# Kernel tuning notes

Hardware: AMD Instinct MI355X
Metric: run time of the kernel (lower is better)

The kernel has to match this reference:

```python
import jax, jax.numpy as jnp
import numpy as np

B, S, T, D, H, HID, V, O = 8, 512, 256, 768, 12, 3072, 50257, 64
HD = D // H  # head dim = 64


def setup_inputs() -> dict:
    key = jax.random.key(0)
    ks = jax.random.split(key, 20)
    s = 0.02
    return {
        'source_input_ids': jax.random.randint(ks[0], (B, S), 0, V, dtype=jnp.int32),
        'encoder_hidden_states': jax.random.normal(ks[1], (B, S, D), dtype=jnp.float32),
        'encoder_attn_mask': jnp.zeros((B, S), dtype=bool),
        'decoder_hidden_states': jax.random.normal(ks[2], (B, T, D), dtype=jnp.float32),
        'onto_ids': jnp.arange(V - O, V, dtype=jnp.int32),
        # MultiheadAttention params (torch layout: W [out,in])
        'Wq': jax.random.normal(ks[3], (D, D)) * s, 'bq': jnp.zeros((D,)),
        'Wk': jax.random.normal(ks[4], (D, D)) * s, 'bk': jnp.zeros((D,)),
        'Wv': jax.random.normal(ks[5], (D, D)) * s, 'bv': jnp.zeros((D,)),
        'Wo': jax.random.normal(ks[6], (D, D)) * s, 'bo': jnp.zeros((D,)),
        # CopyHead: Linear(D, 1)
        'copy_w': jax.random.normal(ks[7], (D, 1)) * s, 'copy_b': jnp.zeros((1,)),
        # Generator FFN: Linear(D, HID) -> relu -> Linear(HID, O)
        'W1': jax.random.normal(ks[8], (HID, D)) * s, 'b1': jnp.zeros((HID,)),
        'W2': jax.random.normal(ks[9], (O, HID)) * s, 'b2': jnp.zeros((O,)),
    }


def _forward(source_input_ids, encoder_hidden_states, encoder_attn_mask,
             decoder_hidden_states, onto_ids, Wq, bq, Wk, bk, Wv, bv, Wo, bo,
             copy_w, copy_b, W1, b1, W2, b2):
    # ---- Generator: FFN + softmax over ontology vocab ----
    h = jax.nn.relu(decoder_hidden_states @ W1.T + b1)
    ontology_probs = jax.nn.softmax(h @ W2.T + b2, axis=-1)  # [B,T,O]

    # ---- MultiheadAttention (batch_first, eval: no dropout) ----
    q = (decoder_hidden_states @ Wq.T + bq).reshape(B, T, H, HD)
    k = (encoder_hidden_states @ Wk.T + bk).reshape(B, S, H, HD)
    v = (encoder_hidden_states @ Wv.T + bv).reshape(B, S, H, HD)
    scores = jnp.einsum('bthd,bshd->bhts', q, k) / jnp.sqrt(jnp.float32(HD))
    scores = jnp.where(encoder_attn_mask[:, None, None, :], -jnp.inf, scores)
    attn = jax.nn.softmax(scores, axis=-1)                       # [B,H,T,S]
    ctx = jnp.einsum('bhts,bshd->bthd', attn, v).reshape(B, T, D)
    context_outputs = ctx @ Wo.T + bo                            # [B,T,D]
    from_source_probs = attn.mean(axis=1)                        # avg heads [B,T,S]

    # ---- CopyHead ----
    copy_probs = jax.nn.sigmoid(context_outputs @ copy_w + copy_b)  # [B,T,1]

    from_source_probs = from_source_probs * copy_probs
    ontology_probs = ontology_probs * (1.0 - copy_probs)

    # ---- scatter-add into full vocab distribution ----
    bi = jnp.arange(B)[:, None, None]
    ti = jnp.arange(T)[None, :, None]
    vocab_probs = jnp.zeros((B, T, V), dtype=copy_probs.dtype)
    vocab_probs = vocab_probs.at[bi, ti, source_input_ids[:, None, :]].add(from_source_probs)
    vocab_probs = vocab_probs.at[bi, ti, onto_ids[None, None, :]].add(ontology_probs)
    return vocab_probs


def reference(source_input_ids, encoder_hidden_states, encoder_attn_mask,
              decoder_hidden_states, onto_ids, Wq, bq, Wk, bk, Wv, bv, Wo, bo,
              copy_w, copy_b, W1, b1, W2, b2):
    return _forward(source_input_ids, encoder_hidden_states, encoder_attn_mask,
                    decoder_hidden_states, onto_ids, Wq, bq, Wk, bk, Wv, bv,
                    Wo, bo, copy_w, copy_b, W1, b1, W2, b2)
```

## Files before the change

kernel.cpp:

```cpp
#include <hip/hip_runtime.h>
#include <hip/hip_bf16.h>
#include <math.h>

constexpr int B = 8, S = 512, T = 256, D = 768, H = 12, HID = 3072;
constexpr int V = 50257, O = 64, HD = 64;

typedef short bf16x8 __attribute__((ext_vector_type(8)));
typedef float f32x4 __attribute__((ext_vector_type(4)));

__device__ __forceinline__ float b2f(unsigned short u) {
  union { float f; unsigned v; } x; x.v = ((unsigned)u) << 16; return x.f;
}
__device__ __forceinline__ unsigned short f2b(float f) {
  __hip_bfloat16 h = __float2bfloat16(f);
  return *(unsigned short*)&h;
}

__device__ __forceinline__ void async16(const void* g, void* l) {
  __builtin_amdgcn_global_load_lds(
      (const __attribute__((address_space(1))) void*)g,
      (__attribute__((address_space(3))) void*)l, 16, 0, 0);
}

constexpr int CH0 = B * T * D / 8;
constexpr int CH1 = CH0 + B * S * D / 8;
constexpr int CH2 = CH1 + HID * D / 8;
constexpr int CH3 = CH2 + D * D / 8;
constexpr int CH4 = CH3 + D * D / 8;
constexpr int CH5 = CH4 + D * D / 8;
constexpr int CH6 = CH5 + O * HID / 8;

__global__ void cvt_weff_kernel(
    const float* __restrict__ dec, const float* __restrict__ enc,
    const float* __restrict__ W1, const float* __restrict__ Wq,
    const float* __restrict__ Wk, const float* __restrict__ Wv,
    const float* __restrict__ W2, const float* __restrict__ Wo,
    const float* __restrict__ bo, const float* __restrict__ cw,
    const float* __restrict__ cb,
    __hip_bfloat16* __restrict__ decb, __hip_bfloat16* __restrict__ encb,
    __hip_bfloat16* __restrict__ WA, __hip_bfloat16* __restrict__ WB,
    __hip_bfloat16* __restrict__ W2b, float* __restrict__ weff) {
  int i = blockIdx.x * blockDim.x + threadIdx.x;
  if (i >= CH6) {
    int j = i - CH6;
    if (j < D) {
      float acc = 0.f;
      for (int o = 0; o < D; ++o) acc += Wo[(size_t)o * D + j] * cw[o];
      weff[j] = acc;
    } else if (j == D) {
      float acc = cb[0];
      for (int o = 0; o < D; ++o) acc += bo[o] * cw[o];
      weff[D] = acc;
    }
    return;
  }
  const float* src;
  __hip_bfloat16* dst;
  int j;
  if (i < CH0)      { src = dec; dst = decb;                 j = i; }
  else if (i < CH1) { src = enc; dst = encb;                 j = i - CH0; }
  else if (i < CH2) { src = W1;  dst = WA;                   j = i - CH1; }
  else if (i < CH3) { src = Wq;  dst = WA + (size_t)HID * D; j = i - CH2; }
  else if (i < CH4) { src = Wk;  dst = WB;                   j = i - CH3; }
  else if (i < CH5) { src = Wv;  dst = WB + (size_t)D * D;   j = i - CH4; }
  else              { src = W2;  dst = W2b;                  j = i - CH5; }
  size_t e = (size_t)j * 8;
  float4 v0 = *(const float4*)&src[e];
  float4 v1 = *(const float4*)&src[e + 4];
  ushort4 o0, o1;
  o0.x = f2b(v0.x); o0.y = f2b(v0.y); o0.z = f2b(v0.z); o0.w = f2b(v0.w);
  o1.x = f2b(v1.x); o1.y = f2b(v1.y); o1.z = f2b(v1.z); o1.w = f2b(v1.w);
  *(ushort4*)&dst[e] = o0;
  *(ushort4*)&dst[e + 4] = o1;
}

__device__ __forceinline__ void zero_range(float* out, long long lo4,
                                           long long hi4, int zb, int nzb) {
  f32x4* o4 = (f32x4*)out;
  const f32x4 z = {0.f, 0.f, 0.f, 0.f};
  for (long long i = lo4 + (long long)zb * 256 + threadIdx.x; i < hi4;
       i += (long long)nzb * 256)
    __builtin_nontemporal_store(z, &o4[i]);
}

constexpr long long OUT_N4 = (long long)B * T * V / 4;
constexpr long long HALF4 = OUT_N4 / 2;

template <int BN, int MODE>
__device__ __forceinline__ void gemm_body(
    const __hip_bfloat16* __restrict__ A, const __hip_bfloat16* __restrict__ W,
    const float* __restrict__ bias0, const float* __restrict__ bias1,
    float* __restrict__ Cf, __hip_bfloat16* __restrict__ out0,
    __hip_bfloat16* __restrict__ out1, int M, int N, int K,
    int bx, int by, int kbeg, int kend,
    __hip_bfloat16* Als, __hip_bfloat16* Bls) {
  constexpr int BK = 32;
  constexpr int WTN = BN / 2;
  constexpr int NFRAG = WTN / 16;
  const int tid = threadIdx.x;
  const int lane = tid & 63, wid = tid >> 6;
  const int wm = wid >> 1, wn = wid & 1;
  const int row0 = by * 128, col0 = bx * BN;
  const int lr = lane & 15;
  const int ko = (lane >> 4) * 8;

  f32x4 acc[4][NFRAG] = {};

  for (int k0 = kbeg; k0 < kend; k0 += BK) {
#pragma unroll
    for (int c = 0; c < 2; ++c) {
      int j = tid + c * 256;
      int r = j >> 2, col = (j & 3) * 8;
      async16(&A[(size_t)(row0 + r) * K + k0 + col], (void*)&Als[j * 8]);
    }
#pragma unroll
    for (int c = 0; c < BN / 64; ++c) {
      int j = tid + c * 256;
      int r = j >> 2, col = (j & 3) * 8;
      async16(&W[(size_t)(col0 + r) * K + k0 + col], (void*)&Bls[j * 8]);
    }
    __syncthreads();

    bf16x8 af[4], bfr[NFRAG];
#pragma unroll
    for (int mi = 0; mi < 4; ++mi)
      af[mi] = *(const bf16x8*)&Als[(wm * 64 + mi * 16 + lr) * BK + ko];
#pragma unroll
    for (int ni = 0; ni < NFRAG; ++ni)
      bfr[ni] = *(const bf16x8*)&Bls[(wn * WTN + ni * 16 + lr) * BK + ko];
#pragma unroll
    for (int mi = 0; mi < 4; ++mi)
#pragma unroll
      for (int ni = 0; ni < NFRAG; ++ni)
        acc[mi][ni] = __builtin_amdgcn_mfma_f32_16x16x32_bf16(
            af[mi], bfr[ni], acc[mi][ni], 0, 0, 0);
    __syncthreads();
  }

#pragma unroll
  for (int mi = 0; mi < 4; ++mi) {
    int rbase = row0 + wm * 64 + mi * 16 + (lane >> 4) * 4;
#pragma unroll
    for (int ni = 0; ni < NFRAG; ++ni) {
      int c = col0 + wn * WTN + ni * 16 + lr;
#pragma unroll
      for (int r = 0; r < 4; ++r) {
        int rr = rbase + r;
        float a = acc[mi][ni][r];
        if constexpr (MODE == 1) {
          if (c < HID) {
            out0[(size_t)rr * HID + c] = __float2bfloat16(fmaxf(a + bias0[c], 0.f));
          } else {
            out1[(size_t)rr * D + (c - HID)] = __float2bfloat16(a + bias1[c - HID]);
          }
        } else if constexpr (MODE == 2) {
          if (c < D) {
            out0[(size_t)rr * D + c] = __float2bfloat16(a + bias0[c]);
          } else {
            int d = c - D;
            size_t idx = (((size_t)(rr >> 9) * D + d) << 9) | (size_t)(rr & 511);
            out1[idx] = __float2bfloat16(a + bias1[d]);
          }
        } else {
          Cf[(size_t)rr * N + c] = a;
        }
      }
    }
  }
}

constexpr int KV_BX = (2 * D) / 128;
constexpr int KV_BLOCKS = KV_BX * (B * S / 128);
constexpr int FQ_BX = (HID + D) / 128;
constexpr int FQ_BLOCKS = FQ_BX * (B * T / 128);
constexpr int GEMM_BLOCKS = KV_BLOCKS + FQ_BLOCKS;
constexpr int Z1 = 1024;

__global__ __launch_bounds__(256) void gemm_mega_kernel(
    const __hip_bfloat16* __restrict__ encb, const __hip_bfloat16* __restrict__ WB,
    const float* __restrict__ bk, const float* __restrict__ bv,
    __hip_bfloat16* __restrict__ kb16, __hip_bfloat16* __restrict__ vt,
    const __hip_bfloat16* __restrict__ decb, const __hip_bfloat16* __restrict__ WA,
    const float* __restrict__ b1, const float* __restrict__ bq,
    __hip_bfloat16* __restrict__ hb16, __hip_bfloat16* __restrict__ qb16,
    float* __restrict__ out) {
  __shared__ __hip_bfloat16 Als[128 * 32];
  __shared__ __hip_bfloat16 Bls[128 * 32];
  int bid = blockIdx.x;
  if (bid < KV_BLOCKS) {
    gemm_body<128, 2>(encb, WB, bk, bv, nullptr, kb16, vt,
                      B * S, 2 * D, D, bid % KV_BX, bid / KV_BX, 0, D, Als, Bls);
  } else if (bid < GEMM_BLOCKS) {
    int r = bid - KV_BLOCKS;
    gemm_body<128, 1>(decb, WA, b1, bq, nullptr, hb16, qb16,
                      B * T, HID + D, D, r % FQ_BX, r / FQ_BX, 0, D, Als, Bls);
  } else {
    zero_range(out, 0, HALF4, bid - GEMM_BLOCKS, Z1);
  }
}

constexpr int NSPLIT = 16;
constexpr int KCH = HID / NSPLIT;
constexpr int FFN2_BLOCKS = NSPLIT * (B * T / 128);

constexpr int ATTN_BLOCKS = B * H * (T / 32);
constexpr int Z2 = 1024;

__device__ void attn_body(
    const __hip_bfloat16* __restrict__ q, const __hip_bfloat16* __restrict__ k,
    const __hip_bfloat16* __restrict__ vt, const unsigned char* __restrict__ mask,
    __hip_bfloat16* __restrict__ ctx, __hip_bfloat16* __restrict__ Pg,
    int bid, char* smem) {
  constexpr int TB = 32;
  constexpr int SCP = 520;
  __hip_bfloat16* Qls = (__hip_bfloat16*)smem;
  __hip_bfloat16* KVls = Qls + TB * 64;
  __hip_bfloat16* sc = KVls + 128 * 64;
  const int tid = threadIdx.x;
  const int lane = tid & 63, w = tid >> 6;
  const int lr = lane & 15, lg = lane >> 4;
  const int tile = bid & 7;
  const int h = (bid >> 3) % H;
  const int b = bid / (8 * H);
  const int t0 = tile * TB;

  {
    int r = tid >> 3, slot = tid & 7;
    int g = slot ^ (r & 7);
    async16(&q[((size_t)(b * T + t0 + r)) * D + h * 64 + g * 8],
            (void*)&Qls[tid * 8]);
  }

  for (int ch = 0; ch < 4; ++ch) {
    const int s0 = ch * 128;
#pragma unroll
    for (int it = 0; it < 4; ++it) {
      int c = tid + it * 256;
      int r = c >> 3, slot = c & 7;
      int g = slot ^ (r & 7);
      async16(&k[((size_t)(b * S + s0 + r)) * D + h * 64 + g * 8],
              (void*)&KVls[c * 8]);
    }
    __syncthreads();
    f32x4 acc[2][2] = {};
#pragma unroll
    for (int ks = 0; ks < 2; ++ks) {
      bf16x8 af[2], bfr[2];
#pragma unroll
      for (int mi = 0; mi < 2; ++mi) {
        int row = mi * 16 + lr;
        int slot = (4 * ks + lg) ^ (row & 7);
        af[mi] = *(const bf16x8*)&Qls[row * 64 + slot * 8];
      }
#pragma unroll
      for (int ni = 0; ni < 2; ++ni) {
        int row = w * 32 + ni * 16 + lr;
        int slot = (4 * ks + lg) ^ (row & 7);
        bfr[ni] = *(const bf16x8*)&KVls[row * 64 + slot * 8];
      }
#pragma unroll
      for (int mi = 0; mi < 2; ++mi)
#pragma unroll
        for (int ni = 0; ni < 2; ++ni)
          acc[mi][ni] = __builtin_amdgcn_mfma_f32_16x16x32_bf16(
              af[mi], bfr[ni], acc[mi][ni], 0, 0, 0);
    }
#pragma unroll
    for (int ni = 0; ni < 2; ++ni) {
      int s_local = w * 32 + ni * 16 + lr;
      bool msk = mask[b * S + s0 + s_local];
#pragma unroll
      for (int mi = 0; mi < 2; ++mi) {
        int trow = mi * 16 + lg * 4;
#pragma unroll
        for (int rg = 0; rg < 4; ++rg) {
          float val = msk ? -INFINITY : acc[mi][ni][rg] * 0.125f;
          sc[(trow + rg) * SCP + s0 + s_local] = __float2bfloat16(val);
        }
      }
    }
    __syncthreads();
  }

  unsigned short* scu = (unsigned short*)sc;
  unsigned short* pgu = (unsigned short*)Pg;
#pragma unroll
  for (int i = 0; i < 8; ++i) {
    int r = w * 8 + i;
    float x[8];
    float m = -INFINITY;
#pragma unroll
    for (int j = 0; j < 8; ++j) {
      x[j] = b2f(scu[r * SCP + j * 64 + lane]);
      m = fmaxf(m, x[j]);
    }
#pragma unroll
    for (int o = 32; o > 0; o >>= 1) m = fmaxf(m, __shfl_xor(m, o));
    float ssum = 0.f;
#pragma unroll
    for (int j = 0; j < 8; ++j) { x[j] = __expf(x[j] - m); ssum += x[j]; }
#pragma unroll
    for (int o = 32; o > 0; o >>= 1) ssum += __shfl_xor(ssum, o);
    float inv = 1.f / ssum;
#pragma unroll
    for (int j = 0; j < 8; ++j) {
      unsigned short pb = f2b(x[j] * inv);
      scu[r * SCP + j * 64 + lane] = pb;
      pgu[(((size_t)(b * H + h)) * T + t0 + r) * S + j * 64 + lane] = pb;
    }
  }
  __syncthreads();

  f32x4 accp[2] = {};
  for (int ch = 0; ch < 4; ++ch) {
    const int s0 = ch * 128;
#pragma unroll
    for (int it = 0; it < 4; ++it) {
      int c = tid + it * 256;
      int d = c >> 4, slot = c & 15;
      int g = slot ^ (d & 7);
      async16(&vt[(((size_t)(b * H + h)) * 64 + d) * S + s0 + g * 8],
              (void*)&KVls[c * 8]);
    }
    __syncthreads();
#pragma unroll
    for (int ks = 0; ks < 4; ++ks) {
      bf16x8 bfr;
      {
        int brow = w * 16 + lr;
        int slot = (4 * ks + lg) ^ (brow & 7);
        bfr = *(const bf16x8*)&KVls[brow * 128 + slot * 8];
      }
#pragma unroll
      for (int mi = 0; mi < 2; ++mi) {
        int prow = mi * 16 + lr;
        bf16x8 af = *(const bf16x8*)&sc[prow * SCP + s0 + ks * 32 + lg * 8];
        accp[mi] = __builtin_amdgcn_mfma_f32_16x16x32_bf16(af, bfr, accp[mi], 0, 0, 0);
      }
    }
    __syncthreads();
  }
#pragma unroll
  for (int mi = 0; mi < 2; ++mi) {
    int trow = mi * 16 + lg * 4;
#pragma unroll
    for (int rg = 0; rg < 4; ++rg) {
      ctx[((size_t)(b * T + t0 + trow + rg)) * D + h * 64 + w * 16 + lr] =
          __float2bfloat16(accp[mi][rg]);
    }
  }
}

__global__ __launch_bounds__(256) void attn_ffn2_kernel(
    const __hip_bfloat16* __restrict__ q, const __hip_bfloat16* __restrict__ k,
    const __hip_bfloat16* __restrict__ vt, const unsigned char* __restrict__ mask,
    __hip_bfloat16* __restrict__ ctx, __hip_bfloat16* __restrict__ Pg,
    const __hip_bfloat16* __restrict__ hb16, const __hip_bfloat16* __restrict__ W2b,
    float* __restrict__ part, float* __restrict__ out) {
  __shared__ __align__(16) char smem[53760];
  int bid = blockIdx.x;
  if (bid < ATTN_BLOCKS) {
    attn_body(q, k, vt, mask, ctx, Pg, bid, smem);
  } else if (bid < ATTN_BLOCKS + FFN2_BLOCKS) {
    int r = bid - ATTN_BLOCKS;
    int sp = r & (NSPLIT - 1), mt = r / NSPLIT;
    __hip_bfloat16* Als = (__hip_bfloat16*)smem;
    __hip_bfloat16* Bls = Als + 128 * 32;
    gemm_body<64, 3>(hb16, W2b, nullptr, nullptr,
                     part + (size_t)sp * (B * T) * 64, nullptr, nullptr,
                     B * T, 64, HID, 0, mt, sp * KCH, (sp + 1) * KCH, Als, Bls);
  } else {
    zero_range(out, HALF4, OUT_N4, bid - ATTN_BLOCKS - FFN2_BLOCKS, Z2);
  }
}

__global__ __launch_bounds__(256) void scatter3_kernel(
    const int* __restrict__ src, const int* __restrict__ onto,
    const __hip_bfloat16* __restrict__ Pg, const float* __restrict__ part,
    const float* __restrict__ b2v, const __hip_bfloat16* __restrict__ ctx,
    const float* __restrict__ weff, float* __restrict__ out) {
  const int bt = blockIdx.x;
  const int b = bt >> 8, t = bt & (T - 1);
  const int tid = threadIdx.x;
  const int lane = tid & 63;
  float* row = out + (size_t)bt * V;

  __shared__ float red[256];
  __shared__ float onts[O];

  const unsigned short* cu = (const unsigned short*)ctx + (size_t)bt * D;
  float a = 0.f;
#pragma unroll
  for (int j = 0; j < 3; ++j) {
    int d = j * 256 + tid;
    a += b2f(cu[d]) * weff[d];
  }
  red[tid] = a;
  __syncthreads();
  for (int st = 128; st > 0; st >>= 1) {
    if (tid < st) red[tid] += red[tid + st];
    __syncthreads();
  }
  const float cpv = 1.f / (1.f + __expf(-(red[0] + weff[D])));
  __syncthreads();

  if (tid < 64) {
    float x = b2v[lane];
#pragma unroll
    for (int sp = 0; sp < NSPLIT; ++sp)
      x += part[((size_t)sp * (B * T) + bt) * 64 + lane];
    float m = x;
#pragma unroll
    for (int o = 32; o > 0; o >>= 1) m = fmaxf(m, __shfl_xor(m, o));
    float e = __expf(x - m);
    float ss = e;
#pragma unroll
    for (int o = 32; o > 0; o >>= 1) ss += __shfl_xor(ss, o);
    onts[lane] = e / ss * (1.f - cpv);
  }
  __syncthreads();

  const unsigned short* pg = (const unsigned short*)Pg;
#pragma unroll
  for (int jj = 0; jj < 2; ++jj) {
    int s = jj * 256 + tid;
    float sum = 0.f;
#pragma unroll
    for (int h = 0; h < H; ++h)
      sum += b2f(pg[(((size_t)(b * H + h)) * T + t) * S + s]);
    atomicAdd(&row[src[b * S + s]], sum * (1.0f / (float)H) * cpv);
  }
  if (tid < O) atomicAdd(&row[onto[tid]], onts[tid]);
}

extern "C" void kernel_launch(void* const* d_in, const int* in_sizes, int n_in,
                              void* d_out, int out_size, void* d_ws, size_t ws_size,
                              hipStream_t stream) {
  const int* src_ids = (const int*)d_in[0];
  const float* enc = (const float*)d_in[1];
  const unsigned char* mask = (const unsigned char*)d_in[2];
  const float* dec = (const float*)d_in[3];
  const int* onto_ids = (const int*)d_in[4];
  const float* Wq = (const float*)d_in[5];
  const float* bq = (const float*)d_in[6];
  const float* Wk = (const float*)d_in[7];
  const float* bk = (const float*)d_in[8];
  const float* Wv = (const float*)d_in[9];
  const float* bv = (const float*)d_in[10];
  const float* Wo = (const float*)d_in[11];
  const float* bo = (const float*)d_in[12];
  const float* copy_w = (const float*)d_in[13];
  const float* copy_b = (const float*)d_in[14];
  const float* W1 = (const float*)d_in[15];
  const float* b1 = (const float*)d_in[16];
  const float* W2 = (const float*)d_in[17];
  const float* b2 = (const float*)d_in[18];

  const int MT = B * T;
  const int MS = B * S;

  __hip_bfloat16* wb = (__hip_bfloat16*)d_ws;
  __hip_bfloat16* qb16 = wb;    wb += (size_t)MT * D;
  __hip_bfloat16* kb16 = wb;    wb += (size_t)MS * D;
  __hip_bfloat16* vt = wb;      wb += (size_t)MS * D;
  __hip_bfloat16* ctxb16 = wb;  wb += (size_t)MT * D;
  __hip_bfloat16* W2b = wb;     wb += (size_t)O * HID;
  __hip_bfloat16* WB = wb;      wb += (size_t)2 * D * D;
  __hip_bfloat16* WA = wb;      wb += (size_t)(HID + D) * D;
  __hip_bfloat16* hb16 = wb;    wb += (size_t)MT * HID;
  __hip_bfloat16* Pg = wb;
  __hip_bfloat16* decb = wb;
  __hip_bfloat16* encb = decb + (size_t)MT * D;
  wb += (size_t)B * H * T * S;
  float* wf = (float*)wb;
  float* part = wf;             wf += (size_t)NSPLIT * MT * O;
  float* weff = wf;             wf += (size_t)(D + 1);

  float* out = (float*)d_out;

  cvt_weff_kernel<<<CH6 / 256 + 4, 256, 0, stream>>>(
      dec, enc, W1, Wq, Wk, Wv, W2, Wo, bo, copy_w, copy_b,
      decb, encb, WA, WB, W2b, weff);

  gemm_mega_kernel<<<GEMM_BLOCKS + Z1, 256, 0, stream>>>(
      encb, WB, bk, bv, kb16, vt, decb, WA, b1, bq, hb16, qb16, out);

  attn_ffn2_kernel<<<ATTN_BLOCKS + FFN2_BLOCKS + Z2, 256, 0, stream>>>(
      qb16, kb16, vt, mask, ctxb16, Pg, hb16, W2b, part, out);

  scatter3_kernel<<<MT, 256, 0, stream>>>(
      src_ids, onto_ids, Pg, part, b2, ctxb16, weff, out);
}
```

Measured before the change: 282.7 us.

## Move output zeroing into scatter kernel and swizzle block order for XCD locality

The output is no longer zeroed by extra blocks appended to the GEMM and attention kernels. Each scatter block now zeroes its own vocab row just before scattering into it, so that row is written while still warm in cache. The GEMM and attention block indices are remapped with an XCD-style swizzle so that neighbouring tiles land on the same chiplet and share its L2. FFN2 blocks are also moved ahead of attention in the launch order. The risk is that the zeroing, about 400 MB of stores, now sits on the scatter kernel's critical path instead of overlapping with compute, and the stores are no longer nontemporal.

```diff
diff --git a/kernel.cpp b/kernel.cpp
--- a/kernel.cpp
+++ b/kernel.cpp
@@ -74,18 +74,6 @@
   *(ushort4*)&dst[e + 4] = o1;
 }
 
-__device__ __forceinline__ void zero_range(float* out, long long lo4,
-                                           long long hi4, int zb, int nzb) {
-  f32x4* o4 = (f32x4*)out;
-  const f32x4 z = {0.f, 0.f, 0.f, 0.f};
-  for (long long i = lo4 + (long long)zb * 256 + threadIdx.x; i < hi4;
-       i += (long long)nzb * 256)
-    __builtin_nontemporal_store(z, &o4[i]);
-}
-
-constexpr long long OUT_N4 = (long long)B * T * V / 4;
-constexpr long long HALF4 = OUT_N4 / 2;
-
 template <int BN, int MODE>
 __device__ __forceinline__ void gemm_body(
     const __hip_bfloat16* __restrict__ A, const __hip_bfloat16* __restrict__ W,
@@ -174,7 +162,6 @@
 constexpr int FQ_BX = (HID + D) / 128;
 constexpr int FQ_BLOCKS = FQ_BX * (B * T / 128);
 constexpr int GEMM_BLOCKS = KV_BLOCKS + FQ_BLOCKS;
-constexpr int Z1 = 1024;
 
 __global__ __launch_bounds__(256) void gemm_mega_kernel(
     const __hip_bfloat16* __restrict__ encb, const __hip_bfloat16* __restrict__ WB,
@@ -182,20 +169,18 @@
     __hip_bfloat16* __restrict__ kb16, __hip_bfloat16* __restrict__ vt,
     const __hip_bfloat16* __restrict__ decb, const __hip_bfloat16* __restrict__ WA,
     const float* __restrict__ b1, const float* __restrict__ bq,
-    __hip_bfloat16* __restrict__ hb16, __hip_bfloat16* __restrict__ qb16,
-    float* __restrict__ out) {
+    __hip_bfloat16* __restrict__ hb16, __hip_bfloat16* __restrict__ qb16) {
   __shared__ __hip_bfloat16 Als[128 * 32];
   __shared__ __hip_bfloat16 Bls[128 * 32];
   int bid = blockIdx.x;
-  if (bid < KV_BLOCKS) {
+  int gid = (bid & 7) * (GEMM_BLOCKS / 8) + (bid >> 3);
+  if (gid < KV_BLOCKS) {
     gemm_body<128, 2>(encb, WB, bk, bv, nullptr, kb16, vt,
-                      B * S, 2 * D, D, bid % KV_BX, bid / KV_BX, 0, D, Als, Bls);
-  } else if (bid < GEMM_BLOCKS) {
-    int r = bid - KV_BLOCKS;
+                      B * S, 2 * D, D, gid % KV_BX, gid / KV_BX, 0, D, Als, Bls);
+  } else {
+    int r = gid - KV_BLOCKS;
     gemm_body<128, 1>(decb, WA, b1, bq, nullptr, hb16, qb16,
                       B * T, HID + D, D, r % FQ_BX, r / FQ_BX, 0, D, Als, Bls);
-  } else {
-    zero_range(out, 0, HALF4, bid - GEMM_BLOCKS, Z1);
   }
 }
 
@@ -204,7 +189,6 @@
 constexpr int FFN2_BLOCKS = NSPLIT * (B * T / 128);
 
 constexpr int ATTN_BLOCKS = B * H * (T / 32);
-constexpr int Z2 = 1024;
 
 __device__ void attn_body(
     const __hip_bfloat16* __restrict__ q, const __hip_bfloat16* __restrict__ k,
@@ -356,25 +340,24 @@
     const __hip_bfloat16* __restrict__ vt, const unsigned char* __restrict__ mask,
     __hip_bfloat16* __restrict__ ctx, __hip_bfloat16* __restrict__ Pg,
     const __hip_bfloat16* __restrict__ hb16, const __hip_bfloat16* __restrict__ W2b,
-    float* __restrict__ part, float* __restrict__ out) {
+    float* __restrict__ part) {
   __shared__ __align__(16) char smem[53760];
   int bid = blockIdx.x;
-  if (bid < ATTN_BLOCKS) {
-    attn_body(q, k, vt, mask, ctx, Pg, bid, smem);
-  } else if (bid < ATTN_BLOCKS + FFN2_BLOCKS) {
-    int r = bid - ATTN_BLOCKS;
-    int sp = r & (NSPLIT - 1), mt = r / NSPLIT;
+  if (bid < FFN2_BLOCKS) {
+    int sp = bid & (NSPLIT - 1), mt = bid / NSPLIT;
     __hip_bfloat16* Als = (__hip_bfloat16*)smem;
     __hip_bfloat16* Bls = Als + 128 * 32;
     gemm_body<64, 3>(hb16, W2b, nullptr, nullptr,
                      part + (size_t)sp * (B * T) * 64, nullptr, nullptr,
                      B * T, 64, HID, 0, mt, sp * KCH, (sp + 1) * KCH, Als, Bls);
   } else {
-    zero_range(out, HALF4, OUT_N4, bid - ATTN_BLOCKS - FFN2_BLOCKS, Z2);
-  }
-}
-
-__global__ __launch_bounds__(256) void scatter3_kernel(
+    int r = bid - FFN2_BLOCKS;
+    int aid = (r & 7) * (ATTN_BLOCKS / 8) + (r >> 3);
+    attn_body(q, k, vt, mask, ctx, Pg, aid, smem);
+  }
+}
+
+__global__ __launch_bounds__(256) void scatter4_kernel(
     const int* __restrict__ src, const int* __restrict__ onto,
     const __hip_bfloat16* __restrict__ Pg, const float* __restrict__ part,
     const float* __restrict__ b2v, const __hip_bfloat16* __restrict__ ctx,
@@ -387,6 +370,18 @@
 
   __shared__ float red[256];
   __shared__ float onts[O];
+
+  {
+    uintptr_t addr = (uintptr_t)row;
+    int head = (int)(((16 - (addr & 15)) & 15) >> 2);
+    if (tid < head) row[tid] = 0.f;
+    int n4 = (V - head) >> 2;
+    f32x4* row4 = (f32x4*)(row + head);
+    const f32x4 z = {0.f, 0.f, 0.f, 0.f};
+    for (int i = tid; i < n4; i += 256) row4[i] = z;
+    int tail0 = head + (n4 << 2);
+    if (tid < V - tail0) row[tail0 + tid] = 0.f;
+  }
 
   const unsigned short* cu = (const unsigned short*)ctx + (size_t)bt * D;
   float a = 0.f;
@@ -482,12 +477,12 @@
       dec, enc, W1, Wq, Wk, Wv, W2, Wo, bo, copy_w, copy_b,
       decb, encb, WA, WB, W2b, weff);
 
-  gemm_mega_kernel<<<GEMM_BLOCKS + Z1, 256, 0, stream>>>(
-      encb, WB, bk, bv, kb16, vt, decb, WA, b1, bq, hb16, qb16, out);
-
-  attn_ffn2_kernel<<<ATTN_BLOCKS + FFN2_BLOCKS + Z2, 256, 0, stream>>>(
-      qb16, kb16, vt, mask, ctxb16, Pg, hb16, W2b, part, out);
-
-  scatter3_kernel<<<MT, 256, 0, stream>>>(
+  gemm_mega_kernel<<<GEMM_BLOCKS, 256, 0, stream>>>(
+      encb, WB, bk, bv, kb16, vt, decb, WA, b1, bq, hb16, qb16);
+
+  attn_ffn2_kernel<<<FFN2_BLOCKS + ATTN_BLOCKS, 256, 0, stream>>>(
+      qb16, kb16, vt, mask, ctxb16, Pg, hb16, W2b, part);
+
+  scatter4_kernel<<<MT, 256, 0, stream>>>(
       src_ids, onto_ids, Pg, part, b2, ctxb16, weff, out);
 }
```

After: 303.1 us. 7.2% more time.
